# Optimization experiments

Hardware: AMD Instinct MI355X
Metric: run time of the kernel (lower is better)

Reference implementation:

```python
import jax, jax.numpy as jnp
import numpy as np

H = 1024
A = H // 2
B = 32
S = 1024
T = 1024


def setup_inputs() -> dict:
    key = jax.random.key(0)
    ks = jax.random.split(key, 16)
    sc = 0.02
    inp = {
        "hidden": jax.random.normal(ks[0], (1, B, H), jnp.float32),
        "encoder_hiddens": jax.random.normal(ks[1], (S, B, H), jnp.float32),
        "h0_s": jax.random.normal(ks[2], (T, B, H), jnp.float32),
        "ax": jax.random.uniform(ks[3], (B, S, 1), jnp.float32),
        # weights: torch Linear(in,out,bias=False) -> W has shape [out,in], y = x @ W.T
        "W1": jax.random.normal(ks[4], (A, H), jnp.float32) * sc,
        "W2": jax.random.normal(ks[5], (A, H), jnp.float32) * sc,
        "W3": jax.random.normal(ks[6], (A, 1), jnp.float32) * sc,
        "W4": jax.random.normal(ks[7], (1, 3 * A), jnp.float32) * sc,
        "W5": jax.random.normal(ks[8], (A, H), jnp.float32) * sc,
        "W6": jax.random.normal(ks[9], (A, H), jnp.float32) * sc,
        "W7": jax.random.normal(ks[10], (A, H), jnp.float32) * sc,
        "W8": jax.random.normal(ks[11], (1, 3 * A), jnp.float32) * sc,
        "W9": jax.random.normal(ks[12], (H, H), jnp.float32) * sc,
        "W10": jax.random.normal(ks[13], (H, H), jnp.float32) * sc,
        "W11": jax.random.normal(ks[14], (1, 2 * H), jnp.float32) * sc,
    }
    return inp


def reference(hidden, encoder_hiddens, h0_s, ax,
              W1, W2, W3, W4, W5, W6, W7, W8, W9, W10, W11):
    h = hidden[0]  # [B,H], hidden.squeeze(0)

    # ---- encoder (x) attention with coverage, vectorized over S ----
    wx = jnp.einsum('sbh,ah->sba', encoder_hiddens, W1)          # [S,B,A]
    wxy = h @ W2.T                                               # [B,A]
    # Linear3 on ax[:, j] ([B,1]): outer product with W3 column
    wxr = ax[:, :, 0][:, :, None] * W3[:, 0][None, None, :]       # [B,S,A]
    wxr = jnp.transpose(wxr, (1, 0, 2))                           # [S,B,A]
    cat_x = jnp.tanh(jnp.concatenate(
        [wx, jnp.broadcast_to(wxy, (S,) + wxy.shape), wxr], axis=-1))  # [S,B,3A]
    exi = jnp.einsum('sbc,oc->bso', cat_x, W4)                    # [B,S,1]
    axi = jax.nn.softmax(exi, axis=1)                             # [B,S,1]
    cxi = jnp.einsum('bs,sbh->bh', axi[:, :, 0], encoder_hiddens)  # [B,H]
    ax_new = ax + axi

    # ---- decoder-history (t) attention, vectorized over T ----
    wt = jnp.einsum('tbh,ah->tba', h0_s, W5)                      # [T,B,A]
    wtx = cxi @ W6.T                                              # [B,A]
    wty = h @ W7.T                                                # [B,A]
    Tn = h0_s.shape[0]
    cat_t = jnp.tanh(jnp.concatenate(
        [wt,
         jnp.broadcast_to(wtx, (Tn,) + wtx.shape),
         jnp.broadcast_to(wty, (Tn,) + wty.shape)], axis=-1))     # [T,B,3A]
    eti = jnp.einsum('tbc,oc->bto', cat_t, W8)                    # [B,T,1]
    ati = jax.nn.softmax(eti, axis=1)
    cti = jnp.einsum('bt,tbh->bh', ati[:, :, 0], h0_s)            # [B,H]

    # ---- gated fusion ----
    gxi = jnp.tanh(cxi @ W9.T)
    gti = jnp.tanh(cti @ W10.T)
    zi = jax.nn.sigmoid(jnp.concatenate([cxi, cti], axis=1) @ W11.T)  # [B,1]
    ci = zi * gxi + (1.0 - zi) * gti                              # [B,H]
    return ci, ax_new
```

## Files before the change

kernel.cpp:

```cpp
#include <hip/hip_runtime.h>
#include <hip/hip_bf16.h>

#define HH 1024
#define AA 512
#define BB 32
#define SS 1024
#define TN 1024
#define M_ENC (SS*BB)
#define M_TOT ((SS+TN)*BB)
#define NCH 8

#define ABUF 4096

typedef __attribute__((ext_vector_type(8))) short short8;
typedef __attribute__((ext_vector_type(4))) float f4;

union bfu { __hip_bfloat16 h; unsigned short u; };
__device__ __forceinline__ unsigned int f2bu(float x) {
  bfu t; t.h = __float2bfloat16(x); return (unsigned int)t.u;
}
__device__ __forceinline__ unsigned short f2b(float x) {
  bfu t; t.h = __float2bfloat16(x); return t.u;
}
__device__ __forceinline__ float tanh_fast(float x) {
  float e = __expf(2.f * x);
  return 1.f - 2.f / (e + 1.f);
}

__global__ void wprep(const float* __restrict__ W, unsigned short* __restrict__ Wc) {
  const int t = blockIdx.x * 256 + threadIdx.x;
  const int lane = t & 63;
  const int rg = (t >> 6) & 31;
  const int kb = t >> 11;
  const int row = rg * 16 + (lane & 15);
  const int k = kb * 32 + ((lane >> 4) << 3);
  const float* src = W + (size_t)row * HH + k;
  f4 v0 = *(const f4*)(src);
  f4 v1 = *(const f4*)(src + 4);
  short8 o;
  o[0] = f2b(v0[0]); o[1] = f2b(v0[1]); o[2] = f2b(v0[2]); o[3] = f2b(v0[3]);
  o[4] = f2b(v1[0]); o[5] = f2b(v1[1]); o[6] = f2b(v1[2]); o[7] = f2b(v1[3]);
  *(short8*)(Wc + (size_t)t * 8) = o;
}

__global__ void poly_prep(const float* __restrict__ W3, const float* __restrict__ W4,
                          float* __restrict__ C) {
  __shared__ float r1[AA], r3[AA], r5[AA];
  const int a = threadIdx.x;
  const float w = W3[a], u = W4[2 * AA + a];
  const float w2 = w * w;
  r1[a] = u * w;
  r3[a] = u * w * w2;
  r5[a] = u * w * w2 * w2;
  __syncthreads();
  for (int off = 256; off > 0; off >>= 1) {
    if (a < off) { r1[a] += r1[a + off]; r3[a] += r3[a + off]; r5[a] += r5[a + off]; }
    __syncthreads();
  }
  if (a == 0) { C[0] = r1[0]; C[1] = -r3[0] / 3.f; C[2] = r5[0] * (2.f / 15.f); }
}

__global__ __launch_bounds__(512, 4)
void e1_gemm(const float* __restrict__ enc, const float* __restrict__ h0,
             const unsigned short* __restrict__ W1c, const unsigned short* __restrict__ W5c,
             const float* __restrict__ W4, const float* __restrict__ W8,
             float* __restrict__ e1s, float* __restrict__ e1t) {
  const int wg   = blockIdx.x;
  const int tid  = threadIdx.x;
  const int lane = tid & 63;
  const int colg = tid >> 6;
  const int l15  = lane & 15;
  const int lg   = lane >> 4;

  const bool is_enc = (wg * 64) < M_ENC;
  const float* __restrict__ Xg = is_enc ? enc : h0;
  const unsigned short* __restrict__ Wc = is_enc ? W1c : W5c;
  const float* __restrict__ Vg = is_enc ? W4 : W8;
  const int row0 = is_enc ? wg * 64 : wg * 64 - M_ENC;

  __shared__ char lds_raw[2 * ABUF];
  float* lred = (float*)lds_raw;

  f4 acc[4][4];
#pragma unroll
  for (int i = 0; i < 4; ++i)
#pragma unroll
    for (int j = 0; j < 4; ++j) acc[i][j] = (f4){0.f, 0.f, 0.f, 0.f};

  const int arow = tid >> 3;
  const int aq   = tid & 7;
  const float* ap = Xg + (size_t)(row0 + arow) * HH + aq * 4;
  const int slotS = (aq >> 1) ^ ((arow >> 1) & 3);
  const int aDst = arow * 64 + slotS * 16 + (aq & 1) * 8;

  const int aRd = l15 * 64 + ((lg ^ ((l15 >> 1) & 3)) << 4);

  const char* bp = (const char*)Wc + colg * 4096 + lane * 16;

  f4 an;
  short8 bA[4], bB[4];

#define ALOAD() do { an = *(const f4*)ap; ap += 32; } while (0)

#define BLOAD(dst) do {                                                       \
    dst[0] = *(const short8*)(bp);                                            \
    dst[1] = *(const short8*)(bp + 1024);                                     \
    dst[2] = *(const short8*)(bp + 2048);                                     \
    dst[3] = *(const short8*)(bp + 3072);                                     \
    bp += 32768;                                                              \
  } while (0)

#define AWR(bo_) do {                                                         \
    uint2 o_;                                                                 \
    o_.x = f2bu(an[0]) | (f2bu(an[1]) << 16);                                 \
    o_.y = f2bu(an[2]) | (f2bu(an[3]) << 16);                                 \
    *(uint2*)(lds_raw + (bo_) + aDst) = o_;                                   \
  } while (0)

#define COMPUTE(bo_, bfr_) do {                                               \
    const char* base_ = lds_raw + (bo_);                                      \
    __builtin_amdgcn_s_setprio(1);                                            \
    _Pragma("unroll")                                                         \
    for (int rt = 0; rt < 4; ++rt) {                                          \
      short8 af_ = *(const short8*)(base_ + aRd + rt * 1024);                 \
      _Pragma("unroll")                                                       \
      for (int cf = 0; cf < 4; ++cf)                                          \
        acc[rt][cf] = __builtin_amdgcn_mfma_f32_16x16x32_bf16(af_, bfr_[cf],  \
                                                     acc[rt][cf], 0, 0, 0);   \
    }                                                                         \
    __builtin_amdgcn_s_setprio(0);                                            \
  } while (0)

#define SYNCA() do {                                                          \
    __builtin_amdgcn_sched_barrier(0);                                        \
    asm volatile("s_waitcnt lgkmcnt(0)" ::: "memory");                        \
    __builtin_amdgcn_s_barrier();                                             \
    __builtin_amdgcn_sched_barrier(0);                                        \
  } while (0)

  ALOAD();
  AWR(0);
  BLOAD(bA);
  SYNCA();

#pragma unroll 1
  for (int it = 0; it < 15; ++it) {
    ALOAD(); BLOAD(bB);
    COMPUTE(0, bA);
    AWR(ABUF);
    SYNCA();
    ALOAD(); BLOAD(bA);
    COMPUTE(ABUF, bB);
    AWR(0);
    SYNCA();
  }
  ALOAD(); BLOAD(bB);
  COMPUTE(0, bA);
  AWR(ABUF);
  SYNCA();
  COMPUTE(ABUF, bB);
#undef ALOAD
#undef BLOAD
#undef AWR
#undef COMPUTE
#undef SYNCA

  float vvv[4];
#pragma unroll
  for (int cf = 0; cf < 4; ++cf) vvv[cf] = Vg[colg * 64 + cf * 16 + l15];

  __syncthreads();
#pragma unroll
  for (int rt = 0; rt < 4; ++rt) {
    float ps[4] = {0.f, 0.f, 0.f, 0.f};
#pragma unroll
    for (int cf = 0; cf < 4; ++cf) {
      const float w = vvv[cf];
#pragma unroll
      for (int r = 0; r < 4; ++r) ps[r] += w * tanh_fast(acc[rt][cf][r]);
    }
#pragma unroll
    for (int r = 0; r < 4; ++r) {
#pragma unroll
      for (int off = 1; off < 16; off <<= 1) ps[r] += __shfl_xor(ps[r], off);
    }
    if (l15 == 0) {
#pragma unroll
      for (int r = 0; r < 4; ++r)
        lred[colg * 64 + rt * 16 + lg * 4 + r] = ps[r];
    }
  }
  __syncthreads();
  if (tid < 64) {
    float s = 0.f;
#pragma unroll
    for (int c = 0; c < 8; ++c) s += lred[c * 64 + tid];
    const int gr = row0 + tid;
    const int q = gr >> 5;
    const int b = gr & 31;
    if (is_enc) e1s[b * SS + q] = s;
    else        e1t[b * TN + q] = s;
  }
}

__global__ void softmax_bs(const float* __restrict__ e1s, const float* __restrict__ ax,
                           const float* __restrict__ C,
                           float* __restrict__ wout, float* __restrict__ axnew) {
  const int b = blockIdx.x, tid = threadIdx.x;
  const float c0 = C[0], c1 = C[1], c2 = C[2];
  __shared__ float red[256];
  float loc[4], xv[4];
  float m = -1e30f;
#pragma unroll
  for (int i = 0; i < 4; ++i) {
    const int s = i * 256 + tid;
    const float x = ax[b * SS + s];
    const float x2 = x * x;
    xv[i] = x;
    loc[i] = e1s[b * SS + s] + x * (c0 + x2 * (c1 + x2 * c2));
    m = fmaxf(m, loc[i]);
  }
  red[tid] = m; __syncthreads();
  for (int off = 128; off > 0; off >>= 1) {
    if (tid < off) red[tid] = fmaxf(red[tid], red[tid + off]);
    __syncthreads();
  }
  m = red[0]; __syncthreads();
  float sum = 0.f;
#pragma unroll
  for (int i = 0; i < 4; ++i) { loc[i] = __expf(loc[i] - m); sum += loc[i]; }
  red[tid] = sum; __syncthreads();
  for (int off = 128; off > 0; off >>= 1) {
    if (tid < off) red[tid] += red[tid + off];
    __syncthreads();
  }
  const float inv = 1.f / red[0];
#pragma unroll
  for (int i = 0; i < 4; ++i) {
    const int s = i * 256 + tid;
    const float a_ = loc[i] * inv;
    wout[b * SS + s] = a_;
    axnew[b * SS + s] = xv[i] + a_;
  }
}

__global__ void softmax_tb(const float* __restrict__ e1t, float* __restrict__ wout) {
  const int b = blockIdx.x, tid = threadIdx.x;
  __shared__ float red[256];
  float loc[4];
  float m = -1e30f;
#pragma unroll
  for (int i = 0; i < 4; ++i) { loc[i] = e1t[b * TN + i * 256 + tid]; m = fmaxf(m, loc[i]); }
  red[tid] = m; __syncthreads();
  for (int off = 128; off > 0; off >>= 1) {
    if (tid < off) red[tid] = fmaxf(red[tid], red[tid + off]);
    __syncthreads();
  }
  m = red[0]; __syncthreads();
  float sum = 0.f;
#pragma unroll
  for (int i = 0; i < 4; ++i) { loc[i] = __expf(loc[i] - m); sum += loc[i]; }
  red[tid] = sum; __syncthreads();
  for (int off = 128; off > 0; off >>= 1) {
    if (tid < off) red[tid] += red[tid + off];
    __syncthreads();
  }
  const float inv = 1.f / red[0];
#pragma unroll
  for (int i = 0; i < 4; ++i) wout[b * TN + (i * 256 + tid)] = loc[i] * inv;
}

__global__ void wpart(const float* __restrict__ X, const float* __restrict__ w,
                      float* __restrict__ part) {
  const int b = blockIdx.x / NCH, ch = blockIdx.x % NCH;
  const int tid = threadIdx.x;
  __shared__ float ws[SS / NCH];
  if (tid < SS / NCH) ws[tid] = w[b * SS + ch * (SS / NCH) + tid];
  __syncthreads();
  f4 acc = (f4){0.f, 0.f, 0.f, 0.f};
  const float* base = X + ((size_t)(ch * (SS / NCH)) * BB + b) * HH + tid * 4;
#pragma unroll 4
  for (int i = 0; i < SS / NCH; ++i) {
    f4 x = *(const f4*)(base + (size_t)i * BB * HH);
    acc += ws[i] * x;
  }
  *(f4*)&part[((size_t)(b * NCH + ch)) * HH + tid * 4] = acc;
}

__global__ void wreduce(const float* __restrict__ part, float* __restrict__ out) {
  const int idx = blockIdx.x * 256 + threadIdx.x;
  const int b = idx / HH, h = idx % HH;
  float s = 0.f;
#pragma unroll
  for (int ch = 0; ch < NCH; ++ch) s += part[((size_t)(b * NCH + ch)) * HH + h];
  out[idx] = s;
}

__global__ void zi_kernel(const float* __restrict__ cxi, const float* __restrict__ cti,
                          const float* __restrict__ W11, float* __restrict__ zi) {
  const int b = blockIdx.x, tid = threadIdx.x;
  float s = 0.f;
  for (int i = tid; i < HH; i += 256) s += cxi[b * HH + i] * W11[i] + cti[b * HH + i] * W11[HH + i];
  __shared__ float red[4];
  for (int off = 32; off > 0; off >>= 1) s += __shfl_down(s, off);
  if ((tid & 63) == 0) red[tid >> 6] = s;
  __syncthreads();
  if (tid == 0) {
    float t = red[0] + red[1] + red[2] + red[3];
    zi[b] = 1.f / (1.f + __expf(-t));
  }
}

__global__ void ci_kernel(const float* __restrict__ cxi, const float* __restrict__ cti,
                          const float* __restrict__ W9, const float* __restrict__ W10,
                          const float* __restrict__ zi, float* __restrict__ out_ci) {
  const int b = blockIdx.x >> 2, hb = blockIdx.x & 3, tid = threadIdx.x;
  const int h = hb * 256 + tid;
  __shared__ float cx[HH], ct[HH];
  for (int i = tid; i < HH; i += 256) { cx[i] = cxi[b * HH + i]; ct[i] = cti[b * HH + i]; }
  __syncthreads();
  const float* __restrict__ w9r  = W9  + (size_t)h * HH;
  const float* __restrict__ w10r = W10 + (size_t)h * HH;
  float gx = 0.f, gt = 0.f;
  for (int k = 0; k < HH; k += 4) {
    f4 a = *(const f4*)(w9r + k);
    f4 c = *(const f4*)(w10r + k);
    gx += cx[k] * a[0] + cx[k + 1] * a[1] + cx[k + 2] * a[2] + cx[k + 3] * a[3];
    gt += ct[k] * c[0] + ct[k + 1] * c[1] + ct[k + 2] * c[2] + ct[k + 3] * c[3];
  }
  const float z = zi[b];
  out_ci[b * HH + h] = z * tanhf(gx) + (1.f - z) * tanhf(gt);
}

extern "C" void kernel_launch(void* const* d_in, const int* in_sizes, int n_in,
                              void* d_out, int out_size, void* d_ws, size_t ws_size,
                              hipStream_t stream) {
  const float* enc = (const float*)d_in[1];
  const float* h0  = (const float*)d_in[2];
  const float* ax  = (const float*)d_in[3];
  const float* W1  = (const float*)d_in[4];
  const float* W3  = (const float*)d_in[6];
  const float* W4  = (const float*)d_in[7];
  const float* W5  = (const float*)d_in[8];
  const float* W8  = (const float*)d_in[11];
  const float* W9  = (const float*)d_in[12];
  const float* W10 = (const float*)d_in[13];
  const float* W11 = (const float*)d_in[14];
  float* out = (float*)d_out;

  float* w = (float*)d_ws;
  unsigned short* W1c = (unsigned short*)w;
  unsigned short* W5c = (unsigned short*)(w + 262144);
  float* partx = w;
  float* partt = w + 262144;
  float* e1s   = w + 524288;
  float* e1t   = w + 557056;
  float* axi   = w + 589824;
  float* ati   = w + 622592;
  float* cxi   = w + 655360;
  float* cti   = w + 688128;
  float* zi    = w + 720896;
  float* Cpoly = w + 720960;

  wprep<<<256, 256, 0, stream>>>(W1, W1c);
  wprep<<<256, 256, 0, stream>>>(W5, W5c);
  poly_prep<<<1, 512, 0, stream>>>(W3, W4, Cpoly);
  e1_gemm<<<M_TOT / 64, 512, 0, stream>>>(enc, h0, W1c, W5c, W4, W8, e1s, e1t);
  softmax_bs<<<BB, 256, 0, stream>>>(e1s, ax, Cpoly, axi, out + BB * HH);
  softmax_tb<<<BB, 256, 0, stream>>>(e1t, ati);
  wpart<<<BB * NCH, 256, 0, stream>>>(enc, axi, partx);
  wpart<<<BB * NCH, 256, 0, stream>>>(h0, ati, partt);
  wreduce<<<BB * HH / 256, 256, 0, stream>>>(partx, cxi);
  wreduce<<<BB * HH / 256, 256, 0, stream>>>(partt, cti);
  zi_kernel<<<BB, 256, 0, stream>>>(cxi, cti, W11, zi);
  ci_kernel<<<BB * 4, 256, 0, stream>>>(cxi, cti, W9, W10, zi, out);
}
```

Measured before the change: 224.5 us.

## Double K-step per barrier in fused projection GEMM mainloop

Each pipeline stage of the GEMM mainloop now covers two 32-wide K slices instead of one. That halves the number of LDS barriers, and the LDS A buffer grows to 8 KB per stage. A-tile global loads are issued one stage ahead. The B fragments, now eight per stage, are loaded just before compute instead of being double-buffered in registers. This cuts sync overhead but may expose B load latency and raises register pressure.

```diff
diff --git a/kernel.cpp b/kernel.cpp
--- a/kernel.cpp
+++ b/kernel.cpp
@@ -10,7 +10,7 @@
 #define M_TOT ((SS+TN)*BB)
 #define NCH 8
 
-#define ABUF 4096
+#define ABUF 8192
 
 typedef __attribute__((ext_vector_type(8))) short short8;
 typedef __attribute__((ext_vector_type(4))) float f4;
@@ -97,38 +97,46 @@
 
   const char* bp = (const char*)Wc + colg * 4096 + lane * 16;
 
-  f4 an;
-  short8 bA[4], bB[4];
-
-#define ALOAD() do { an = *(const f4*)ap; ap += 32; } while (0)
-
-#define BLOAD(dst) do {                                                       \
-    dst[0] = *(const short8*)(bp);                                            \
-    dst[1] = *(const short8*)(bp + 1024);                                     \
-    dst[2] = *(const short8*)(bp + 2048);                                     \
-    dst[3] = *(const short8*)(bp + 3072);                                     \
-    bp += 32768;                                                              \
+  f4 an0, an1;
+  short8 bfr[8];
+
+#define ALOAD(k_) do {                                                        \
+    an0 = *(const f4*)(ap + (k_) * 64);                                       \
+    an1 = *(const f4*)(ap + (k_) * 64 + 32);                                  \
   } while (0)
 
 #define AWR(bo_) do {                                                         \
-    uint2 o_;                                                                 \
-    o_.x = f2bu(an[0]) | (f2bu(an[1]) << 16);                                 \
-    o_.y = f2bu(an[2]) | (f2bu(an[3]) << 16);                                 \
-    *(uint2*)(lds_raw + (bo_) + aDst) = o_;                                   \
-  } while (0)
-
-#define COMPUTE(bo_, bfr_) do {                                               \
+    uint2 o0_, o1_;                                                           \
+    o0_.x = f2bu(an0[0]) | (f2bu(an0[1]) << 16);                              \
+    o0_.y = f2bu(an0[2]) | (f2bu(an0[3]) << 16);                              \
+    o1_.x = f2bu(an1[0]) | (f2bu(an1[1]) << 16);                              \
+    o1_.y = f2bu(an1[2]) | (f2bu(an1[3]) << 16);                              \
+    *(uint2*)(lds_raw + (bo_) + aDst) = o0_;                                  \
+    *(uint2*)(lds_raw + (bo_) + 4096 + aDst) = o1_;                           \
+  } while (0)
+
+#define BLOAD(kb2_) do {                                                      \
+    const char* b_ = bp + (size_t)(kb2_) * 65536;                             \
+    _Pragma("unroll")                                                         \
+    for (int q_ = 0; q_ < 8; ++q_)                                            \
+      bfr[q_] = *(const short8*)(b_ + (q_ >> 2) * 32768 + (q_ & 3) * 1024);   \
+  } while (0)
+
+#define COMPUTE(bo_) do {                                                     \
     const char* base_ = lds_raw + (bo_);                                      \
-    __builtin_amdgcn_s_setprio(1);                                            \
     _Pragma("unroll")                                                         \
-    for (int rt = 0; rt < 4; ++rt) {                                          \
-      short8 af_ = *(const short8*)(base_ + aRd + rt * 1024);                 \
+    for (int ks_ = 0; ks_ < 2; ++ks_) {                                       \
+      __builtin_amdgcn_s_setprio(1);                                          \
       _Pragma("unroll")                                                       \
-      for (int cf = 0; cf < 4; ++cf)                                          \
-        acc[rt][cf] = __builtin_amdgcn_mfma_f32_16x16x32_bf16(af_, bfr_[cf],  \
-                                                     acc[rt][cf], 0, 0, 0);   \
+      for (int rt = 0; rt < 4; ++rt) {                                        \
+        short8 af_ = *(const short8*)(base_ + ks_ * 4096 + aRd + rt * 1024);  \
+        _Pragma("unroll")                                                     \
+        for (int cf = 0; cf < 4; ++cf)                                        \
+          acc[rt][cf] = __builtin_amdgcn_mfma_f32_16x16x32_bf16(              \
+              af_, bfr[ks_ * 4 + cf], acc[rt][cf], 0, 0, 0);                  \
+      }                                                                       \
+      __builtin_amdgcn_s_setprio(0);                                          \
     }                                                                         \
-    __builtin_amdgcn_s_setprio(0);                                            \
   } while (0)
 
 #define SYNCA() do {                                                          \
@@ -138,30 +146,21 @@
     __builtin_amdgcn_sched_barrier(0);                                        \
   } while (0)
 
-  ALOAD();
+  ALOAD(0);
   AWR(0);
-  BLOAD(bA);
+  ALOAD(1);
   SYNCA();
 
 #pragma unroll 1
-  for (int it = 0; it < 15; ++it) {
-    ALOAD(); BLOAD(bB);
-    COMPUTE(0, bA);
-    AWR(ABUF);
-    SYNCA();
-    ALOAD(); BLOAD(bA);
-    COMPUTE(ABUF, bB);
-    AWR(0);
-    SYNCA();
-  }
-  ALOAD(); BLOAD(bB);
-  COMPUTE(0, bA);
-  AWR(ABUF);
-  SYNCA();
-  COMPUTE(ABUF, bB);
+  for (int it = 0; it < 7; ++it) {
+    AWR(ABUF); ALOAD(2 * it + 2); BLOAD(2 * it); COMPUTE(0); SYNCA();
+    AWR(0); ALOAD(2 * it + 3); BLOAD(2 * it + 1); COMPUTE(ABUF); SYNCA();
+  }
+  AWR(ABUF); BLOAD(14); COMPUTE(0); SYNCA();
+  BLOAD(15); COMPUTE(ABUF);
 #undef ALOAD
+#undef AWR
 #undef BLOAD
-#undef AWR
 #undef COMPUTE
 #undef SYNCA
 
```

Result: faster. 219.5 us (-2.2%).
